# Kernel optimization log

Hardware: AMD Instinct MI355X
Metric: run time of the kernel (lower is better)

The kernel has to match this reference:

```python
import jax, jax.numpy as jnp
import numpy as np
from jax import lax

N_NODES = 100000
N_EDGES = 1600000
DIM = 64
N_GRAPHS = 128
OUT = 10
BN_EPS = 1e-5


def setup_inputs() -> dict:
    key = jax.random.key(0)
    ks = jax.random.split(key, 8)
    s = 1.0 / np.sqrt(DIM)
    x = jax.random.normal(ks[0], (N_NODES, DIM), dtype=jnp.float32)
    edge_index = jax.random.randint(ks[1], (2, N_EDGES), 0, N_NODES, dtype=jnp.int64)
    batch = jnp.sort(jax.random.randint(ks[2], (N_NODES,), 0, N_GRAPHS, dtype=jnp.int64))
    return {
        "x": x,
        "edge_index": edge_index,
        "batch": batch,
        "W1": jax.random.normal(ks[3], (5, DIM, DIM), dtype=jnp.float32) * s,
        "b1": jnp.zeros((5, DIM), jnp.float32),
        "gamma": jnp.ones((5, DIM), jnp.float32),
        "beta": jnp.zeros((5, DIM), jnp.float32),
        "rmean": jnp.zeros((5, DIM), jnp.float32),
        "rvar": jnp.ones((5, DIM), jnp.float32),
        "W2": jax.random.normal(ks[4], (5, DIM, DIM), dtype=jnp.float32) * s,
        "b2": jnp.zeros((5, DIM), jnp.float32),
        "lin1_w": jax.random.normal(ks[5], (DIM, DIM), dtype=jnp.float32) * s,
        "lin1_b": jnp.zeros((DIM,), jnp.float32),
        "lin2_w": jax.random.normal(ks[6], (DIM, OUT), dtype=jnp.float32) * s,
        "lin2_b": jnp.zeros((OUT,), jnp.float32),
    }


def reference(x, edge_index, batch, W1, b1, gamma, beta, rmean, rvar, W2, b2,
              lin1_w, lin1_b, lin2_w, lin2_b):
    n = x.shape[0]
    src, dst = edge_index[0], edge_index[1]

    def gin_layer(h, p):
        w1, bb1, g, bt, m, v, w2, bb2 = p
        # GINConv (eps=0): h_i <- MLP(h_i + sum_{j in N(i)} h_j)
        agg = jax.ops.segment_sum(h[src], dst, num_segments=n)
        h = h + agg
        h = h @ w1 + bb1
        h = (h - m) * lax.rsqrt(v + BN_EPS) * g + bt  # BatchNorm1d (eval)
        h = jax.nn.relu(h)
        h = jax.nn.relu(h @ w2 + bb2)
        return h, None

    h, _ = lax.scan(gin_layer, x, (W1, b1, gamma, beta, rmean, rvar, W2, b2))
    # global_add_pool over graphs in the batch
    pooled = jax.ops.segment_sum(h, batch, num_segments=N_GRAPHS)  # [G, dim]
    pooled = jax.nn.relu(pooled @ lin1_w + lin1_b)
    # dropout is identity in eval mode
    return pooled @ lin2_w + lin2_b  # [G, out]
```

## Files before the change

### kernel.cpp

```cpp
#include <hip/hip_runtime.h>

#define N_NODES  100000
#define N_EDGES  1600000
#define DIM      64
#define N_GRAPHS 128
#define OUT_DIM  10
#define SCAN_NB    196
#define SCAN_CHUNK 512
#define RANGE_BITS 14
#define RANGE_SIZE 16384
#define N_RANGES   7
#define N_CHUNKS   32
#define CHUNK_EDGES (N_EDGES / N_CHUNKS)
#define NODE_PAD   (N_RANGES * RANGE_SIZE)

typedef unsigned int uint;
typedef unsigned short ushort;
typedef __attribute__((ext_vector_type(8))) short short8;
typedef __attribute__((ext_vector_type(4))) float f32x4;

__device__ __forceinline__ uint f2bf(float x) {
    uint b = __float_as_uint(x);
    b += 0x7fffu + ((b >> 16) & 1u);
    return b >> 16;
}


__global__ __launch_bounds__(1024) void histo_kernel(const int* __restrict__ dst,
                                                     int* __restrict__ counts8) {
    __shared__ int lds[RANGE_SIZE];
    const int c = blockIdx.x & (N_CHUNKS - 1);
    const int r = blockIdx.x >> 5;
    if (r >= N_RANGES) return;
    for (int j = threadIdx.x; j < RANGE_SIZE; j += 1024) lds[j] = 0;
    __syncthreads();
    const int beg = c * CHUNK_EDGES, end = beg + CHUNK_EDGES;
    for (int i0 = beg + threadIdx.x; i0 < end; i0 += 1024 * 8) {
        int d[8];
#pragma unroll
        for (int k = 0; k < 8; ++k) {
            const int i = i0 + k * 1024;
            d[k] = (i < end) ? dst[i] : -1;
        }
#pragma unroll
        for (int k = 0; k < 8; ++k)
            if ((d[k] >> RANGE_BITS) == r) atomicAdd(&lds[d[k] & (RANGE_SIZE - 1)], 1);
    }
    __syncthreads();
    int* outp = counts8 + (c * N_RANGES + r) * RANGE_SIZE;
    for (int j = threadIdx.x; j < RANGE_SIZE; j += 1024) outp[j] = lds[j];
}

__global__ void scanA_kernel(const int* __restrict__ counts8, int* __restrict__ blockSums, int n) {
    __shared__ int red[256];
    const int b = blockIdx.x, t = threadIdx.x;
    int s = 0;
#pragma unroll
    for (int k = 0; k < 2; ++k) {
        const int node = b * SCAN_CHUNK + t * 2 + k;
        if (node < n) {
            const int r = node >> RANGE_BITS, jj = node & (RANGE_SIZE - 1);
            for (int c = 0; c < N_CHUNKS; ++c)
                s += counts8[(c * N_RANGES + r) * RANGE_SIZE + jj];
        }
    }
    red[t] = s;
    __syncthreads();
    for (int off = 128; off > 0; off >>= 1) {
        if (t < off) red[t] += red[t + off];
        __syncthreads();
    }
    if (t == 0) blockSums[b] = red[0];
}

__global__ void scanB_kernel(const int* __restrict__ blockSums, int* __restrict__ blockOffs,
                             int* __restrict__ row_ptr) {
    __shared__ int sc[256];
    const int t = threadIdx.x;
    const int v = (t < SCAN_NB) ? blockSums[t] : 0;
    sc[t] = v;
    __syncthreads();
    for (int off = 1; off < 256; off <<= 1) {
        int u = (t >= off) ? sc[t - off] : 0;
        __syncthreads();
        sc[t] += u;
        __syncthreads();
    }
    if (t < SCAN_NB) blockOffs[t] = sc[t] - v;
    if (t == 255) row_ptr[N_NODES] = sc[255];
}

__global__ void scanC_kernel(const int* __restrict__ counts8, const int* __restrict__ blockOffs,
                             int* __restrict__ row_ptr, int* __restrict__ base8, int n) {
    __shared__ int sc[256];
    const int b = blockIdx.x, t = threadIdx.x;
    const int node0 = b * SCAN_CHUNK + t * 2;
    int cnt0[N_CHUNKS], cnt1[N_CHUNKS];
    int tot0 = 0, tot1 = 0;
    if (node0 < n) {
        const int r = node0 >> RANGE_BITS, jj = node0 & (RANGE_SIZE - 1);
        for (int c = 0; c < N_CHUNKS; ++c) {
            cnt0[c] = counts8[(c * N_RANGES + r) * RANGE_SIZE + jj];
            tot0 += cnt0[c];
        }
    }
    if (node0 + 1 < n) {
        const int r = (node0 + 1) >> RANGE_BITS, jj = (node0 + 1) & (RANGE_SIZE - 1);
        for (int c = 0; c < N_CHUNKS; ++c) {
            cnt1[c] = counts8[(c * N_RANGES + r) * RANGE_SIZE + jj];
            tot1 += cnt1[c];
        }
    }
    const int s = tot0 + tot1;
    sc[t] = s;
    __syncthreads();
    for (int off = 1; off < 256; off <<= 1) {
        int u = (t >= off) ? sc[t - off] : 0;
        __syncthreads();
        sc[t] += u;
        __syncthreads();
    }
    const int pre = blockOffs[b] + sc[t] - s;
    if (node0 < n) {
        row_ptr[node0] = pre;
        int run = pre;
        for (int c = 0; c < N_CHUNKS; ++c) { base8[c * NODE_PAD + node0] = run; run += cnt0[c]; }
    }
    if (node0 + 1 < n) {
        const int pre1 = pre + tot0;
        row_ptr[node0 + 1] = pre1;
        int run = pre1;
        for (int c = 0; c < N_CHUNKS; ++c) { base8[c * NODE_PAD + node0 + 1] = run; run += cnt1[c]; }
    }
}


__global__ __launch_bounds__(1024) void fill_kernel(const int* __restrict__ src,
                                                    const int* __restrict__ dst,
                                                    const int* __restrict__ base8,
                                                    int* __restrict__ col_idx) {
    __shared__ int lds[RANGE_SIZE];
    const int r = blockIdx.x & 7;
    const int c = blockIdx.x >> 3;
    if (r >= N_RANGES) return;
    const int* bp = base8 + c * NODE_PAD + r * RANGE_SIZE;
    for (int j = threadIdx.x; j < RANGE_SIZE; j += 1024)
        lds[j] = __builtin_nontemporal_load(&bp[j]);
    __syncthreads();
    const int beg = c * CHUNK_EDGES, end = beg + CHUNK_EDGES;
    for (int i0 = beg + threadIdx.x; i0 < end; i0 += 1024 * 8) {
        int d[8], s[8];
#pragma unroll
        for (int k = 0; k < 8; ++k) {
            const int i = i0 + k * 1024;
            d[k] = (i < end) ? dst[i] : -1;
            s[k] = (i < end) ? src[i] : 0;
        }
#pragma unroll
        for (int k = 0; k < 8; ++k) {
            if ((d[k] >> RANGE_BITS) == r) {
                int pos = atomicAdd(&lds[d[k] & (RANGE_SIZE - 1)], 1);
                col_idx[pos] = s[k];
            }
        }
    }
}


__global__ void cvt_kernel(const float* __restrict__ x, ushort* __restrict__ xb, int n4) {
    int idx = blockIdx.x * blockDim.x + threadIdx.x;
    if (idx >= n4) return;
    float4 v = ((const float4*)x)[idx];
    uint2 o;
    o.x = f2bf(v.x) | (f2bf(v.y) << 16);
    o.y = f2bf(v.z) | (f2bf(v.w) << 16);
    ((uint2*)xb)[idx] = o;
}


__global__ void repack_kernel(const float* __restrict__ W1, const float* __restrict__ W2,
                              uint4* __restrict__ Wp) {
    const int wave = (blockIdx.x * blockDim.x + threadIdx.x) >> 6;
    if (wave >= 10) return;
    const int layer = wave >> 1;
    const float* W = (wave & 1) ? (W2 + layer * 4096) : (W1 + layer * 4096);
    const int lane = threadIdx.x & 63;
    const int n15 = lane & 15, quad = lane >> 4;
#pragma unroll
    for (int f = 0; f < 8; ++f) {
        const int outer = f >> 1, h = f & 1;
        uint p[4];
#pragma unroll
        for (int pj = 0; pj < 4; ++pj) {
            const int k0 = h * 32 + quad * 8 + 2 * pj;
            uint lo = f2bf(W[k0 * 64 + outer * 16 + n15]);
            uint hi = f2bf(W[(k0 + 1) * 64 + outer * 16 + n15]);
            p[pj] = lo | (hi << 16);
        }
        Wp[(wave * 8 + f) * 64 + lane] = make_uint4(p[0], p[1], p[2], p[3]);
    }
}


__device__ __forceinline__ void add_unpack(float acc[8], uint4 v) {
    acc[0] += __uint_as_float(v.x << 16);
    acc[1] += __uint_as_float(v.x & 0xffff0000u);
    acc[2] += __uint_as_float(v.y << 16);
    acc[3] += __uint_as_float(v.y & 0xffff0000u);
    acc[4] += __uint_as_float(v.z << 16);
    acc[5] += __uint_as_float(v.z & 0xffff0000u);
    acc[6] += __uint_as_float(v.w << 16);
    acc[7] += __uint_as_float(v.w & 0xffff0000u);
}

__global__ __launch_bounds__(256) void layer_kernel(
    const ushort* __restrict__ hbp, ushort* __restrict__ hbn,
    const int* __restrict__ row_ptr, const int* __restrict__ col_idx,
    const uint4* __restrict__ Wp,
    const float* __restrict__ b1, const float* __restrict__ gamma,
    const float* __restrict__ beta, const float* __restrict__ rmean,
    const float* __restrict__ rvar, const float* __restrict__ b2, int ntiles)
{
    __shared__ __align__(16) ushort Ua[4][16][72];
    __shared__ __align__(16) ushort Ub[4][16][72];
    const uint4* __restrict__ hb4 = (const uint4*)hbp;
    const int lane = threadIdx.x & 63;
    const int wid  = threadIdx.x >> 6;
    const int n15  = lane & 15, quad = lane >> 4;
    const int g = lane >> 3;
    const int q = lane & 7;
    const short8* Wp8 = (const short8*)Wp;

    const int tile = blockIdx.x * 4 + wid;
    if (tile >= ntiles) return;
    const int nb = tile * 16;

    for (int ro = 0; ro < 2; ++ro) {
        const int i = nb + ro * 8 + g;
        const int rp0 = row_ptr[i];
        const int rp1 = row_ptr[i + 1];
        float acc[8];
        {
            uint4 v = hb4[(size_t)i * 8 + q];
            acc[0] = __uint_as_float(v.x << 16);
            acc[1] = __uint_as_float(v.x & 0xffff0000u);
            acc[2] = __uint_as_float(v.y << 16);
            acc[3] = __uint_as_float(v.y & 0xffff0000u);
            acc[4] = __uint_as_float(v.z << 16);
            acc[5] = __uint_as_float(v.z & 0xffff0000u);
            acc[6] = __uint_as_float(v.w << 16);
            acc[7] = __uint_as_float(v.w & 0xffff0000u);
        }
        const int nbat = (rp1 - rp0 + 7) >> 3;
        int ixn[8];
#pragma unroll
        for (int k = 0; k < 8; ++k)
            ixn[k] = col_idx[max(min(rp0 + k, rp1 - 1), 0)];
        for (int b = 0; b < nbat; ++b) {
            const int e0 = rp0 + b * 8;
            int ix[8];
#pragma unroll
            for (int k = 0; k < 8; ++k)
                ix[k] = (e0 + k < rp1) ? ixn[k] : N_NODES;
#pragma unroll
            for (int k = 0; k < 8; ++k)
                ixn[k] = col_idx[min(e0 + 8 + k, rp1 - 1)];
            uint4 v[8];
#pragma unroll
            for (int k = 0; k < 8; ++k) v[k] = hb4[(size_t)ix[k] * 8 + q];
#pragma unroll
            for (int k = 0; k < 8; ++k) add_unpack(acc, v[k]);
        }
        uint2 o0, o1;
        o0.x = f2bf(acc[0]) | (f2bf(acc[1]) << 16);
        o0.y = f2bf(acc[2]) | (f2bf(acc[3]) << 16);
        o1.x = f2bf(acc[4]) | (f2bf(acc[5]) << 16);
        o1.y = f2bf(acc[6]) | (f2bf(acc[7]) << 16);
        *(uint2*)&Ua[wid][ro * 8 + g][q * 8]     = o0;
        *(uint2*)&Ua[wid][ro * 8 + g][q * 8 + 4] = o1;
    }
    short8 wf1[8];
#pragma unroll
    for (int f = 0; f < 8; ++f) wf1[f] = Wp8[f * 64 + lane];
    __threadfence_block();

    short8 t0 = *(const short8*)&Ua[wid][n15][quad * 8];
    short8 t1 = *(const short8*)&Ua[wid][n15][32 + quad * 8];
    {
        f32x4 c1[4];
#pragma unroll
        for (int mt = 0; mt < 4; ++mt) {
            c1[mt] = (f32x4){0.f, 0.f, 0.f, 0.f};
            c1[mt] = __builtin_amdgcn_mfma_f32_16x16x32_bf16(wf1[mt * 2 + 0], t0, c1[mt], 0, 0, 0);
            c1[mt] = __builtin_amdgcn_mfma_f32_16x16x32_bf16(wf1[mt * 2 + 1], t1, c1[mt], 0, 0, 0);
        }
#pragma unroll
        for (int mt = 0; mt < 4; ++mt) {
            const int j0 = mt * 16 + quad * 4;
            f32x4 sc, sh;
#pragma unroll
            for (int r = 0; r < 4; ++r) {
                float s = gamma[j0 + r] * rsqrtf(rvar[j0 + r] + 1e-5f);
                sc[r] = s;
                sh[r] = (b1[j0 + r] - rmean[j0 + r]) * s + beta[j0 + r];
            }
            float u0 = fmaxf(c1[mt][0] * sc[0] + sh[0], 0.f);
            float u1 = fmaxf(c1[mt][1] * sc[1] + sh[1], 0.f);
            float u2 = fmaxf(c1[mt][2] * sc[2] + sh[2], 0.f);
            float u3 = fmaxf(c1[mt][3] * sc[3] + sh[3], 0.f);
            uint2 pk;
            pk.x = f2bf(u0) | (f2bf(u1) << 16);
            pk.y = f2bf(u2) | (f2bf(u3) << 16);
            *(uint2*)&Ub[wid][n15][mt * 16 + quad * 4] = pk;
        }
    }
    short8 wf2[8];
#pragma unroll
    for (int f = 0; f < 8; ++f) wf2[f] = Wp8[(8 + f) * 64 + lane];
    __threadfence_block();

    {
        short8 u0 = *(const short8*)&Ub[wid][n15][quad * 8];
        short8 u1 = *(const short8*)&Ub[wid][n15][32 + quad * 8];
        f32x4 c2[4];
#pragma unroll
        for (int tc = 0; tc < 4; ++tc) {
            c2[tc] = (f32x4){0.f, 0.f, 0.f, 0.f};
            c2[tc] = __builtin_amdgcn_mfma_f32_16x16x32_bf16(u0, wf2[tc * 2 + 0], c2[tc], 0, 0, 0);
            c2[tc] = __builtin_amdgcn_mfma_f32_16x16x32_bf16(u1, wf2[tc * 2 + 1], c2[tc], 0, 0, 0);
        }
#pragma unroll
        for (int tc = 0; tc < 4; ++tc) {
            const float bb2 = b2[tc * 16 + n15];
#pragma unroll
            for (int r = 0; r < 4; ++r) {
                float v = fmaxf(c2[tc][r] + bb2, 0.f);
                hbn[(size_t)(nb + quad * 4 + r) * 64 + tc * 16 + n15] = (ushort)f2bf(v);
            }
        }
    }
}


__global__ void pool_kernel(const ushort* __restrict__ hb, const int* __restrict__ batch,
                            float* __restrict__ pooled, int n) {
    const int lane = threadIdx.x & 63;
    const int wid  = threadIdx.x >> 6;
    const int wave = blockIdx.x * 4 + wid;
    const int nwaves = gridDim.x * 4;
    const int per = (n + nwaves - 1) / nwaves;
    const int a = wave * per;
    const int b = min(a + per, n);
    if (a >= b) return;
    int cur = batch[a];
    float sum = 0.0f;
    for (int i = a; i < b; ++i) {
        int g = batch[i];
        if (g != cur) {
            atomicAdd(&pooled[cur * DIM + lane], sum);
            sum = 0.0f;
            cur = g;
        }
        sum += __uint_as_float(((uint)hb[(size_t)i * DIM + lane]) << 16);
    }
    atomicAdd(&pooled[cur * DIM + lane], sum);
}


__global__ void head_kernel(const float* __restrict__ pooled,
                            const float* __restrict__ w1, const float* __restrict__ b1,
                            const float* __restrict__ w2, const float* __restrict__ b2,
                            float* __restrict__ out) {
    const int g = blockIdx.x;
    const int lane = threadIdx.x;
    __shared__ float pl[DIM];
    __shared__ float y1l[DIM];
    pl[lane] = pooled[g * DIM + lane];
    __syncthreads();
    float y = b1[lane];
#pragma unroll
    for (int d = 0; d < DIM; ++d) y += pl[d] * w1[d * DIM + lane];
    y1l[lane] = fmaxf(y, 0.0f);
    __syncthreads();
    if (lane < OUT_DIM) {
        float y2 = b2[lane];
#pragma unroll
        for (int d = 0; d < DIM; ++d) y2 += y1l[d] * w2[d * OUT_DIM + lane];
        out[g * OUT_DIM + lane] = y2;
    }
}


extern "C" void kernel_launch(void* const* d_in, const int* in_sizes, int n_in,
                              void* d_out, int out_size, void* d_ws, size_t ws_size,
                              hipStream_t stream) {
    const float* x     = (const float*)d_in[0];
    const int*   eidx  = (const int*)  d_in[1];
    const int*   batch = (const int*)  d_in[2];
    const float* W1    = (const float*)d_in[3];
    const float* b1    = (const float*)d_in[4];
    const float* gamma = (const float*)d_in[5];
    const float* beta  = (const float*)d_in[6];
    const float* rmean = (const float*)d_in[7];
    const float* rvar  = (const float*)d_in[8];
    const float* W2    = (const float*)d_in[9];
    const float* b2    = (const float*)d_in[10];
    const float* l1w   = (const float*)d_in[11];
    const float* l1b   = (const float*)d_in[12];
    const float* l2w   = (const float*)d_in[13];
    const float* l2b   = (const float*)d_in[14];
    float* out = (float*)d_out;

    const size_t C8 = (size_t)N_CHUNKS * N_RANGES * RANGE_SIZE;
    const size_t B8 = (size_t)N_CHUNKS * NODE_PAD;
    const size_t ROWS = (size_t)N_NODES + 1;
    int* counts8   = (int*)d_ws;
    int* row_ptr   = counts8   + C8;
    int* blockSums = row_ptr   + 100352;
    int* blockOffs = blockSums + 256;
    int* base8     = blockOffs + 256;
    int* col_idx   = base8     + B8;
    uint4* Wp      = (uint4*)(col_idx + 1600000);
    ushort* tb     = (ushort*)(Wp + 5120);
    ushort* hb     = tb + ROWS * DIM;
    float* pooled  = (float*)(hb + ROWS * DIM);

    const int* srcp = eidx;
    const int* dstp = eidx + N_EDGES;

    hipMemsetAsync(pooled, 0, N_GRAPHS * DIM * sizeof(float), stream);
    hipMemsetAsync(tb + (size_t)N_NODES * DIM, 0, DIM * sizeof(ushort), stream);
    hipMemsetAsync(hb + (size_t)N_NODES * DIM, 0, DIM * sizeof(ushort), stream);

    cvt_kernel<<<(N_NODES * DIM / 4 + 255) / 256, 256, 0, stream>>>(x, hb, N_NODES * DIM / 4);
    repack_kernel<<<1, 640, 0, stream>>>(W1, W2, Wp);
    histo_kernel<<<N_CHUNKS * 8, 1024, 0, stream>>>(dstp, counts8);
    scanA_kernel<<<SCAN_NB, 256, 0, stream>>>(counts8, blockSums, N_NODES);
    scanB_kernel<<<1, 256, 0, stream>>>(blockSums, blockOffs, row_ptr);
    scanC_kernel<<<SCAN_NB, 256, 0, stream>>>(counts8, blockOffs, row_ptr, base8, N_NODES);
    fill_kernel<<<N_CHUNKS * 8, 1024, 0, stream>>>(srcp, dstp, base8, col_idx);

    const int ntiles = N_NODES / 16;
    const int layer_blocks = (ntiles + 3) / 4;
    ushort* cur = hb;
    ushort* nxt = tb;
    for (int l = 0; l < 5; ++l) {
        layer_kernel<<<layer_blocks, 256, 0, stream>>>(
            cur, nxt, row_ptr, col_idx, Wp + (size_t)l * 2 * 8 * 64,
            b1 + (size_t)l * DIM, gamma + (size_t)l * DIM, beta + (size_t)l * DIM,
            rmean + (size_t)l * DIM, rvar + (size_t)l * DIM, b2 + (size_t)l * DIM, ntiles);
        ushort* t = cur; cur = nxt; nxt = t;
    }
    pool_kernel<<<2048, 256, 0, stream>>>(cur, batch, pooled, N_NODES);
    head_kernel<<<N_GRAPHS, 64, 0, stream>>>(pooled, l1w, l1b, l2w, l2b, out);
}
```

Before: 345.2 us.

## Replace per-chunk CSR histograms with global atomic counts and global fill cursors

```diff
diff --git a/kernel.cpp b/kernel.cpp
--- a/kernel.cpp
+++ b/kernel.cpp
@@ -10,8 +10,8 @@
 #define RANGE_BITS 14
 #define RANGE_SIZE 16384
 #define N_RANGES   7
-#define N_CHUNKS   32
-#define CHUNK_EDGES (N_EDGES / N_CHUNKS)
+#define N_CHUNKS_F 64
+#define CHUNK_EDGES_F (N_EDGES / N_CHUNKS_F)
 #define NODE_PAD   (N_RANGES * RANGE_SIZE)
 
 typedef unsigned int uint;
@@ -27,14 +27,14 @@
 
 
 __global__ __launch_bounds__(1024) void histo_kernel(const int* __restrict__ dst,
-                                                     int* __restrict__ counts8) {
+                                                     int* __restrict__ counts) {
     __shared__ int lds[RANGE_SIZE];
-    const int c = blockIdx.x & (N_CHUNKS - 1);
-    const int r = blockIdx.x >> 5;
+    const int r = blockIdx.x & 7;
+    const int c = blockIdx.x >> 3;
     if (r >= N_RANGES) return;
     for (int j = threadIdx.x; j < RANGE_SIZE; j += 1024) lds[j] = 0;
     __syncthreads();
-    const int beg = c * CHUNK_EDGES, end = beg + CHUNK_EDGES;
+    const int beg = c * CHUNK_EDGES_F, end = beg + CHUNK_EDGES_F;
     for (int i0 = beg + threadIdx.x; i0 < end; i0 += 1024 * 8) {
         int d[8];
 #pragma unroll
@@ -47,22 +47,21 @@
             if ((d[k] >> RANGE_BITS) == r) atomicAdd(&lds[d[k] & (RANGE_SIZE - 1)], 1);
     }
     __syncthreads();
-    int* outp = counts8 + (c * N_RANGES + r) * RANGE_SIZE;
-    for (int j = threadIdx.x; j < RANGE_SIZE; j += 1024) outp[j] = lds[j];
-}
-
-__global__ void scanA_kernel(const int* __restrict__ counts8, int* __restrict__ blockSums, int n) {
+    int* cnt = counts + r * RANGE_SIZE;
+    for (int j = threadIdx.x; j < RANGE_SIZE; j += 1024) {
+        int v = lds[j];
+        if (v) atomicAdd(&cnt[j], v);
+    }
+}
+
+__global__ void scanA_kernel(const int* __restrict__ counts, int* __restrict__ blockSums, int n) {
     __shared__ int red[256];
     const int b = blockIdx.x, t = threadIdx.x;
     int s = 0;
 #pragma unroll
     for (int k = 0; k < 2; ++k) {
         const int node = b * SCAN_CHUNK + t * 2 + k;
-        if (node < n) {
-            const int r = node >> RANGE_BITS, jj = node & (RANGE_SIZE - 1);
-            for (int c = 0; c < N_CHUNKS; ++c)
-                s += counts8[(c * N_RANGES + r) * RANGE_SIZE + jj];
-        }
+        if (node < n) s += counts[node];
     }
     red[t] = s;
     __syncthreads();
@@ -90,28 +89,14 @@
     if (t == 255) row_ptr[N_NODES] = sc[255];
 }
 
-__global__ void scanC_kernel(const int* __restrict__ counts8, const int* __restrict__ blockOffs,
-                             int* __restrict__ row_ptr, int* __restrict__ base8, int n) {
+__global__ void scanC_kernel(const int* __restrict__ counts, const int* __restrict__ blockOffs,
+                             int* __restrict__ row_ptr, int* __restrict__ cur, int n) {
     __shared__ int sc[256];
     const int b = blockIdx.x, t = threadIdx.x;
     const int node0 = b * SCAN_CHUNK + t * 2;
-    int cnt0[N_CHUNKS], cnt1[N_CHUNKS];
-    int tot0 = 0, tot1 = 0;
-    if (node0 < n) {
-        const int r = node0 >> RANGE_BITS, jj = node0 & (RANGE_SIZE - 1);
-        for (int c = 0; c < N_CHUNKS; ++c) {
-            cnt0[c] = counts8[(c * N_RANGES + r) * RANGE_SIZE + jj];
-            tot0 += cnt0[c];
-        }
-    }
-    if (node0 + 1 < n) {
-        const int r = (node0 + 1) >> RANGE_BITS, jj = (node0 + 1) & (RANGE_SIZE - 1);
-        for (int c = 0; c < N_CHUNKS; ++c) {
-            cnt1[c] = counts8[(c * N_RANGES + r) * RANGE_SIZE + jj];
-            tot1 += cnt1[c];
-        }
-    }
-    const int s = tot0 + tot1;
+    const int c0 = (node0 < n) ? counts[node0] : 0;
+    const int c1 = (node0 + 1 < n) ? counts[node0 + 1] : 0;
+    const int s = c0 + c1;
     sc[t] = s;
     __syncthreads();
     for (int off = 1; off < 256; off <<= 1) {
@@ -121,33 +106,18 @@
         __syncthreads();
     }
     const int pre = blockOffs[b] + sc[t] - s;
-    if (node0 < n) {
-        row_ptr[node0] = pre;
-        int run = pre;
-        for (int c = 0; c < N_CHUNKS; ++c) { base8[c * NODE_PAD + node0] = run; run += cnt0[c]; }
-    }
-    if (node0 + 1 < n) {
-        const int pre1 = pre + tot0;
-        row_ptr[node0 + 1] = pre1;
-        int run = pre1;
-        for (int c = 0; c < N_CHUNKS; ++c) { base8[c * NODE_PAD + node0 + 1] = run; run += cnt1[c]; }
-    }
-}
-
+    if (node0 < n)     { row_ptr[node0] = pre;          cur[node0] = pre; }
+    if (node0 + 1 < n) { row_ptr[node0 + 1] = pre + c0; cur[node0 + 1] = pre + c0; }
+}
 
 __global__ __launch_bounds__(1024) void fill_kernel(const int* __restrict__ src,
                                                     const int* __restrict__ dst,
-                                                    const int* __restrict__ base8,
+                                                    int* __restrict__ cur,
                                                     int* __restrict__ col_idx) {
-    __shared__ int lds[RANGE_SIZE];
     const int r = blockIdx.x & 7;
     const int c = blockIdx.x >> 3;
     if (r >= N_RANGES) return;
-    const int* bp = base8 + c * NODE_PAD + r * RANGE_SIZE;
-    for (int j = threadIdx.x; j < RANGE_SIZE; j += 1024)
-        lds[j] = __builtin_nontemporal_load(&bp[j]);
-    __syncthreads();
-    const int beg = c * CHUNK_EDGES, end = beg + CHUNK_EDGES;
+    const int beg = c * CHUNK_EDGES_F, end = beg + CHUNK_EDGES_F;
     for (int i0 = beg + threadIdx.x; i0 < end; i0 += 1024 * 8) {
         int d[8], s[8];
 #pragma unroll
@@ -159,7 +129,7 @@
 #pragma unroll
         for (int k = 0; k < 8; ++k) {
             if ((d[k] >> RANGE_BITS) == r) {
-                int pos = atomicAdd(&lds[d[k] & (RANGE_SIZE - 1)], 1);
+                int pos = atomicAdd(&cur[d[k]], 1);
                 col_idx[pos] = s[k];
             }
         }
@@ -411,15 +381,13 @@
     const float* l2b   = (const float*)d_in[14];
     float* out = (float*)d_out;
 
-    const size_t C8 = (size_t)N_CHUNKS * N_RANGES * RANGE_SIZE;
-    const size_t B8 = (size_t)N_CHUNKS * NODE_PAD;
     const size_t ROWS = (size_t)N_NODES + 1;
-    int* counts8   = (int*)d_ws;
-    int* row_ptr   = counts8   + C8;
-    int* blockSums = row_ptr   + 100352;
+    int* counts    = (int*)d_ws;
+    int* row_ptr   = counts    + NODE_PAD;
+    int* cur       = row_ptr   + 100352;
+    int* blockSums = cur       + 100352;
     int* blockOffs = blockSums + 256;
-    int* base8     = blockOffs + 256;
-    int* col_idx   = base8     + B8;
+    int* col_idx   = blockOffs + 256;
     uint4* Wp      = (uint4*)(col_idx + 1600000);
     ushort* tb     = (ushort*)(Wp + 5120);
     ushort* hb     = tb + ROWS * DIM;
@@ -428,29 +396,30 @@
     const int* srcp = eidx;
     const int* dstp = eidx + N_EDGES;
 
+    hipMemsetAsync(counts, 0, NODE_PAD * sizeof(int), stream);
     hipMemsetAsync(pooled, 0, N_GRAPHS * DIM * sizeof(float), stream);
     hipMemsetAsync(tb + (size_t)N_NODES * DIM, 0, DIM * sizeof(ushort), stream);
     hipMemsetAsync(hb + (size_t)N_NODES * DIM, 0, DIM * sizeof(ushort), stream);
 
     cvt_kernel<<<(N_NODES * DIM / 4 + 255) / 256, 256, 0, stream>>>(x, hb, N_NODES * DIM / 4);
     repack_kernel<<<1, 640, 0, stream>>>(W1, W2, Wp);
-    histo_kernel<<<N_CHUNKS * 8, 1024, 0, stream>>>(dstp, counts8);
-    scanA_kernel<<<SCAN_NB, 256, 0, stream>>>(counts8, blockSums, N_NODES);
+    histo_kernel<<<N_CHUNKS_F * 8, 1024, 0, stream>>>(dstp, counts);
+    scanA_kernel<<<SCAN_NB, 256, 0, stream>>>(counts, blockSums, N_NODES);
     scanB_kernel<<<1, 256, 0, stream>>>(blockSums, blockOffs, row_ptr);
-    scanC_kernel<<<SCAN_NB, 256, 0, stream>>>(counts8, blockOffs, row_ptr, base8, N_NODES);
-    fill_kernel<<<N_CHUNKS * 8, 1024, 0, stream>>>(srcp, dstp, base8, col_idx);
+    scanC_kernel<<<SCAN_NB, 256, 0, stream>>>(counts, blockOffs, row_ptr, cur, N_NODES);
+    fill_kernel<<<N_CHUNKS_F * 8, 1024, 0, stream>>>(srcp, dstp, cur, col_idx);
 
     const int ntiles = N_NODES / 16;
     const int layer_blocks = (ntiles + 3) / 4;
-    ushort* cur = hb;
-    ushort* nxt = tb;
+    ushort* curb = hb;
+    ushort* nxtb = tb;
     for (int l = 0; l < 5; ++l) {
         layer_kernel<<<layer_blocks, 256, 0, stream>>>(
-            cur, nxt, row_ptr, col_idx, Wp + (size_t)l * 2 * 8 * 64,
+            curb, nxtb, row_ptr, col_idx, Wp + (size_t)l * 2 * 8 * 64,
             b1 + (size_t)l * DIM, gamma + (size_t)l * DIM, beta + (size_t)l * DIM,
             rmean + (size_t)l * DIM, rvar + (size_t)l * DIM, b2 + (size_t)l * DIM, ntiles);
-        ushort* t = cur; cur = nxt; nxt = t;
-    }
-    pool_kernel<<<2048, 256, 0, stream>>>(cur, batch, pooled, N_NODES);
+        ushort* t = curb; curb = nxtb; nxtb = t;
+    }
+    pool_kernel<<<2048, 256, 0, stream>>>(curb, batch, pooled, N_NODES);
     head_kernel<<<N_GRAPHS, 64, 0, stream>>>(pooled, l1w, l1b, l2w, l2b, out);
 }
```

Measured after the change: 404.6 us. 1.17x slower.
